# Optimization experiments

Measured on AMD Instinct MI355X. Metric: run time of the kernel, lower is better.

The kernel has to match this reference:

```python
import jax, jax.numpy as jnp
import numpy as np

BETA = 0.25

def setup_inputs() -> dict:
    key = jax.random.key(0)
    k1, k2 = jax.random.split(key)
    z_e = jax.random.normal(k1, (32, 256, 32, 32), dtype=jnp.float32)
    embed_weight = jax.random.normal(k2, (4096, 256), dtype=jnp.float32) * 0.1
    return {"z_e": z_e, "embed_weight": embed_weight}

def reference(z_e, embed_weight):
    # Eval-mode forward (no input noise, no EMA buffer update).
    B, C, H, W = z_e.shape
    K = embed_weight.shape[0]
    z_t = jnp.transpose(z_e, (0, 2, 3, 1))            # [B,H,W,C]
    z_flat = z_t.reshape(-1, C)                        # [N,C]
    # Squared Euclidean distances; argmin is identical to argmin of cdist(p=2).
    d = (
        jnp.sum(z_flat * z_flat, axis=1, keepdims=True)
        - 2.0 * (z_flat @ embed_weight.T)
        + jnp.sum(embed_weight * embed_weight, axis=1)
    )                                                  # [N,K]
    idx = jnp.argmin(d, axis=1)                        # [N]
    # utilization = (#unique codes used) / vocab_size, jit-safe via bincount-style scatter
    counts = jnp.zeros((K,), dtype=jnp.float32).at[idx].add(1.0)
    utilization = jnp.sum(counts > 0).astype(jnp.float32) / K
    z_q = embed_weight[idx].reshape(B, H, W, C)        # [B,H,W,C]
    commitment_loss = jnp.mean((jax.lax.stop_gradient(z_q) - z_t) ** 2) * BETA
    z_q_st = z_t + jax.lax.stop_gradient(z_q - z_t)    # straight-through
    return jnp.transpose(z_q_st, (0, 3, 1, 2)), commitment_loss, utilization
```

## Files before the change

### kernel.cpp

```cpp
#include <hip/hip_runtime.h>
#include <math.h>


#define WGAP 52

using half8 = __attribute__((ext_vector_type(8))) _Float16;
using f32x4 = __attribute__((ext_vector_type(4))) float;

__device__ __forceinline__ void gload_lds16(const void* g, void* l) {
  __builtin_amdgcn_global_load_lds(
      (const __attribute__((address_space(1))) unsigned int*)g,
      (__attribute__((address_space(3))) unsigned int*)l, 16, 0, 0);
}

__device__ __forceinline__ bool lexlt64(double v, int x, double ov, int ox) {
  return (v < ov) || (v == ov && x < ox);
}

__device__ __forceinline__ void ins3k(int key, int& a0, int& a1, int& a2) {
  const int mx0 = max(key, a0);
  a0 = min(key, a0);
  const int mx1 = max(mx0, a1);
  a1 = min(mx0, a1);
  a2 = min(mx1, a2);
}

__device__ __forceinline__ void mrg3k(int& a0, int& a1, int& a2,
                                      int b0, int b1, int b2) {
  const int c0 = min(a0, b0);
  const int x = max(a0, b0);
  const int y = min(a1, b1);
  const int c1 = min(x, y);
  const int z = max(x, y);
  const int ww = min(a2, b2);
  const int c2 = min(z, ww);
  a0 = c0; a1 = c1; a2 = c2;
}

__global__ __launch_bounds__(256) void vq_prep(const float* __restrict__ E,
                                               uint4* __restrict__ Epk,
                                               float* __restrict__ en1024,
                                               int* __restrict__ used,
                                               double* __restrict__ lossSum,
                                               int* __restrict__ candCount,
                                               int* __restrict__ messyCount) {
  const int t = blockIdx.x * 256 + threadIdx.x;
  if (t < 4096) used[t] = 0;
  if (t == 4096) *lossSum = 0.0;
  if (t == 4097) *candCount = 0;
  if (t == 4098) *messyCount = 0;
  const int code = t >> 5, j = t & 31;
  const int rc = code & 63;
  const int khalf = j >> 4, jo = j & 15;
  const float* src = E + (size_t)code * 256 + j * 8;
  union { half8 h; uint4 u; } pk;
  float s = 0.f;
#pragma unroll
  for (int e = 0; e < 8; ++e) {
    const float z = src[e];
    s = fmaf(z, z, s);
    pk.h[e] = (_Float16)(z * 256.0f);
  }
  const size_t g = (size_t)((code >> 6) * 2 + khalf) * 1024 +
                   rc * 16 + (jo ^ (rc & 15));
  Epk[g] = pk.u;
#pragma unroll
  for (int off = 1; off < 32; off <<= 1) s += __shfl_xor(s, off);
  if (j == 0) en1024[code] = s * 1024.0f;
}

__global__ __launch_bounds__(256, 3) void vq_screen(
    const float* __restrict__ Z, const char* __restrict__ Epk,
    const float* __restrict__ en1024,
    int* __restrict__ pk0, int* __restrict__ pk1, int* __restrict__ pk2) {
  __shared__ char lds[49152];
  const int tid = threadIdx.x;
  const int w = tid >> 6, l = tid & 63;
  const int xcd = blockIdx.x & 7, inner = blockIdx.x >> 3;
  const int part = inner % 3;
  const int qg = (inner / 3) * 8 + xcd;
  const int chs = part * 21 + (part > 0 ? 1 : 0);
  const int che = chs + (part == 0 ? 22 : 21);
  const int S = (che - chs) * 2;
  const int qbase = qg * 128;
  const int b = qbase >> 10;
  const int hwq = (qbase & 1023) + w * 32 + (l & 15);

  const float* Zq = Z + (size_t)b * 262144 + hwq;
  half8 ah[2][8];
#pragma unroll
  for (int u = 0; u < 2; ++u)
#pragma unroll
    for (int ks = 0; ks < 8; ++ks) {
      const int c0 = ks * 32 + (l >> 4) * 8;
#pragma unroll
      for (int e = 0; e < 8; ++e)
        ah[u][ks][e] = (_Float16)(Zq[u * 16 + ((size_t)(c0 + e) << 10)] * 256.0f);
    }

  int lo[4];
#pragma unroll
  for (int s = 0; s < 4; ++s)
    lo[s] = (l & 15) * 256 + (((s * 4 + (l >> 4)) ^ (l & 15)) << 4);

  int k0[2][4], k1[2][4], k2[2][4];
#pragma unroll
  for (int u = 0; u < 2; ++u)
#pragma unroll
    for (int r = 0; r < 4; ++r) {
      k0[u][r] = 0x7fffffff; k1[u][r] = 0x7fffffff; k2[u][r] = 0x7fffffff;
    }

  auto stage = [&](int q) {
    const int ss = chs * 2 + q;
    const char* src = Epk + ((size_t)ss << 14) + w * 4096 + l * 16;
    char* dst = lds + (q % 3) * 16384 + w * 4096;
#pragma unroll
    for (int i = 0; i < 4; ++i) gload_lds16(src + i * 1024, dst + i * 1024);
  };
  stage(0);
  stage(1);

  for (int ch = chs; ch < che; ++ch) {
    f32x4 acc[2][4];
#pragma unroll
    for (int u = 0; u < 2; ++u)
#pragma unroll
      for (int t = 0; t < 4; ++t) acc[u][t] = (f32x4){0.f, 0.f, 0.f, 0.f};

#pragma unroll
    for (int sh = 0; sh < 2; ++sh) {
      const int q = (ch - chs) * 2 + sh;
      if (q + 1 < S) {
        asm volatile("s_waitcnt vmcnt(4)" ::: "memory");
      } else {
        asm volatile("s_waitcnt vmcnt(0)" ::: "memory");
      }
      __builtin_amdgcn_s_barrier();
      __builtin_amdgcn_sched_barrier(0);
      if (q + 2 < S) stage(q + 2);
      const char* Lb = lds + (q % 3) * 16384;
      __builtin_amdgcn_s_setprio(1);
#pragma unroll
      for (int s = 0; s < 4; ++s) {
        const int ks = sh * 4 + s;
#pragma unroll
        for (int t = 0; t < 4; ++t) {
          const half8 eh = *(const half8*)(Lb + t * 4096 + lo[s]);
          acc[0][t] = __builtin_amdgcn_mfma_f32_16x16x32_f16(ah[0][ks], eh, acc[0][t], 0, 0, 0);
          acc[1][t] = __builtin_amdgcn_mfma_f32_16x16x32_f16(ah[1][ks], eh, acc[1][t], 0, 0, 0);
        }
      }
      __builtin_amdgcn_s_setprio(0);
    }

    const int cb = ch * 64;
#pragma unroll
    for (int t = 0; t < 4; ++t) {
      const int code = cb + t * 16 + (l & 15);
      const float en = en1024[code];
#pragma unroll
      for (int u = 0; u < 2; ++u)
#pragma unroll
        for (int r = 0; r < 4; ++r) {
          const float df = fmaf(acc[u][t][r], -0.03125f, en);
          const int di = (int)df;
          const int key = (int)(((unsigned)di << 12) + (unsigned)code);
          ins3k(key, k0[u][r], k1[u][r], k2[u][r]);
        }
    }
  }

#pragma unroll
  for (int mask = 1; mask <= 8; mask <<= 1) {
#pragma unroll
    for (int u = 0; u < 2; ++u)
#pragma unroll
      for (int r = 0; r < 4; ++r) {
        const int o0 = __shfl_xor(k0[u][r], mask);
        const int o1 = __shfl_xor(k1[u][r], mask);
        const int o2 = __shfl_xor(k2[u][r], mask);
        mrg3k(k0[u][r], k1[u][r], k2[u][r], o0, o1, o2);
      }
  }
  if ((l & 15) == 0) {
#pragma unroll
    for (int u = 0; u < 2; ++u)
#pragma unroll
      for (int r = 0; r < 4; ++r) {
        const int n = qbase + w * 32 + u * 16 + (l >> 4) * 4 + r;
        const int o = part * 32768 + n;
        pk0[o] = k0[u][r]; pk1[o] = k1[u][r]; pk2[o] = k2[u][r];
      }
  }
}

__global__ __launch_bounds__(256) void vq_merge(
    const int* __restrict__ pk0, const int* __restrict__ pk1,
    const int* __restrict__ pk2, int* __restrict__ idxOut,
    int* __restrict__ cand, int* __restrict__ candCount,
    int* __restrict__ messy, int* __restrict__ messyCount,
    int* __restrict__ pi0, int* __restrict__ pi1, int* __restrict__ pi2) {
  const int n = blockIdx.x * 256 + threadIdx.x;
  int a0 = pk0[n], a1 = pk1[n], a2 = pk2[n];
#pragma unroll
  for (int q = 1; q < 3; ++q) {
    const int o = q * 32768 + n;
    mrg3k(a0, a1, a2, pk0[o], pk1[o], pk2[o]);
  }
  const int x0 = a0 & 0xfff;
  idxOut[n] = x0;
  const int d0 = a0 >> 12, d1 = a1 >> 12, d2 = a2 >> 12;
  if (d1 - d0 < WGAP) {
    if (d2 - d0 < WGAP) {
      const int p = atomicAdd(messyCount, 1);
      if (p < 4096) messy[p] = n;
    } else {
      const int p = atomicAdd(candCount, 1);
      cand[p] = n;
      pi0[n] = x0; pi1[n] = a1 & 0xfff; pi2[n] = a2 & 0xfff;
    }
  }
}

__global__ __launch_bounds__(256) void vq_cand3(
    const float* __restrict__ Z, const float* __restrict__ E,
    const int* __restrict__ pi0, const int* __restrict__ pi1,
    const int* __restrict__ pi2, const int* __restrict__ cand,
    const int* __restrict__ candCount, int* __restrict__ idxOut) {
  const int w = threadIdx.x >> 6, l = threadIdx.x & 63;
  const int cnt = *candCount;
  for (int j = blockIdx.x * 4 + w; j < cnt; j += gridDim.x * 4) {
    const int n = cand[j];
    const int b = n >> 10, hw = n & 1023;
    const int ca = pi0[n], cbn = pi1[n], cc = pi2[n];
    float z4[4];
#pragma unroll
    for (int i = 0; i < 4; ++i)
      z4[i] = Z[(size_t)b * 262144 + ((size_t)(l * 4 + i) << 10) + hw];
    const float4 e0 = *(const float4*)(E + (size_t)ca * 256 + l * 4);
    const float4 e1 = *(const float4*)(E + (size_t)cbn * 256 + l * 4);
    const float4 e2 = *(const float4*)(E + (size_t)cc * 256 + l * 4);
    double d0 = 0, d1 = 0, d2 = 0;
    const float* p0 = (const float*)&e0;
    const float* p1 = (const float*)&e1;
    const float* p2 = (const float*)&e2;
#pragma unroll
    for (int i = 0; i < 4; ++i) {
      const double f0 = (double)z4[i] - (double)p0[i];
      const double f1 = (double)z4[i] - (double)p1[i];
      const double f2 = (double)z4[i] - (double)p2[i];
      d0 = fma(f0, f0, d0);
      d1 = fma(f1, f1, d1);
      d2 = fma(f2, f2, d2);
    }
#pragma unroll
    for (int off = 32; off > 0; off >>= 1) {
      d0 += __shfl_down(d0, off);
      d1 += __shfl_down(d1, off);
      d2 += __shfl_down(d2, off);
    }
    if (l == 0) {
      double bv = d0; int bx = ca;
      if (lexlt64(d1, cbn, bv, bx)) { bv = d1; bx = cbn; }
      if (lexlt64(d2, cc, bv, bx)) { bv = d2; bx = cc; }
      idxOut[n] = bx;
    }
  }
}

__global__ __launch_bounds__(256) void vq_messy1(
    const float* __restrict__ Z, const float* __restrict__ E,
    const int* __restrict__ messy, const int* __restrict__ messyCount,
    double* __restrict__ parv, int* __restrict__ parx) {
  __shared__ float zs[4][256];
  __shared__ double rv[4][256];
  __shared__ int ri[4][256];
  const int cnt0 = *messyCount;
  const int cnt = cnt0 > 4096 ? 4096 : cnt0;
  const int jobs = ((cnt + 3) >> 2) * 16;
  const int t = threadIdx.x;
  for (int job = blockIdx.x; job < jobs; job += gridDim.x) {
    const int grp = job >> 4, chunk = job & 15;
    __syncthreads();
    {
      const int q = t >> 6, lq = t & 63;
      const int mi = grp * 4 + q;
      const int n = messy[mi < cnt ? mi : grp * 4];
      const int b = n >> 10, hw = n & 1023;
#pragma unroll
      for (int i = 0; i < 4; ++i)
        zs[q][lq * 4 + i] =
            Z[(size_t)b * 262144 + ((size_t)(lq * 4 + i) << 10) + hw];
    }
    __syncthreads();
    const int code = chunk * 256 + t;
    const float* er = E + (size_t)code * 256;
    double s0 = 0, s1 = 0, s2 = 0, s3 = 0;
    for (int c = 0; c < 256; ++c) {
      const double ec = (double)er[c];
      const double f0 = (double)zs[0][c] - ec;
      const double f1 = (double)zs[1][c] - ec;
      const double f2 = (double)zs[2][c] - ec;
      const double f3 = (double)zs[3][c] - ec;
      s0 = fma(f0, f0, s0);
      s1 = fma(f1, f1, s1);
      s2 = fma(f2, f2, s2);
      s3 = fma(f3, f3, s3);
    }
    rv[0][t] = s0; rv[1][t] = s1; rv[2][t] = s2; rv[3][t] = s3;
    ri[0][t] = code; ri[1][t] = code; ri[2][t] = code; ri[3][t] = code;
    __syncthreads();
    for (int s = 128; s > 0; s >>= 1) {
      if (t < s) {
#pragma unroll
        for (int qq = 0; qq < 4; ++qq)
          if (lexlt64(rv[qq][t + s], ri[qq][t + s], rv[qq][t], ri[qq][t])) {
            rv[qq][t] = rv[qq][t + s];
            ri[qq][t] = ri[qq][t + s];
          }
      }
      __syncthreads();
    }
    if (t == 0) {
#pragma unroll
      for (int qq = 0; qq < 4; ++qq) {
        const int mi = grp * 4 + qq;
        if (mi < cnt) {
          parv[mi * 16 + chunk] = rv[qq][0];
          parx[mi * 16 + chunk] = ri[qq][0];
        }
      }
    }
  }
}

__global__ __launch_bounds__(256) void vq_messy2(
    const int* __restrict__ messy, const int* __restrict__ messyCount,
    const double* __restrict__ parv, const int* __restrict__ parx,
    int* __restrict__ idxOut) {
  const int cnt0 = *messyCount;
  const int cnt = cnt0 > 4096 ? 4096 : cnt0;
  for (int j = blockIdx.x * 256 + threadIdx.x; j < cnt; j += gridDim.x * 256) {
    double bv = parv[j * 16];
    int bx = parx[j * 16];
    for (int ch = 1; ch < 16; ++ch) {
      const double v = parv[j * 16 + ch];
      const int x = parx[j * 16 + ch];
      if (lexlt64(v, x, bv, bx)) { bv = v; bx = x; }
    }
    idxOut[messy[j]] = bx;
  }
}

__global__ __launch_bounds__(256) void vq_out(
    const float* __restrict__ Z, const float* __restrict__ E,
    const int* __restrict__ idx, float* __restrict__ out,
    double* __restrict__ lossSum, int* __restrict__ used) {
  __shared__ float zt[32][257];
  __shared__ int ids[32];
  const int tid = threadIdx.x;
  const int qb = blockIdx.x * 32;
  const int b = qb >> 10, hw0 = qb & 1023;
  if (tid < 32) {
    const int id = idx[qb + tid];
    ids[tid] = id;
    used[id] = 1;
  }
  __syncthreads();
  const int w = tid >> 6, l = tid & 63;
#pragma unroll
  for (int rr = 0; rr < 8; ++rr) {
    const int q = rr * 4 + w;
    const float4 v = *(const float4*)(E + (size_t)ids[q] * 256 + l * 4);
    zt[q][l * 4 + 0] = v.x;
    zt[q][l * 4 + 1] = v.y;
    zt[q][l * 4 + 2] = v.z;
    zt[q][l * 4 + 3] = v.w;
  }
  __syncthreads();
  const int hwl = tid & 31, cc = tid >> 5;
  const float* Zb = Z + (size_t)b * 262144 + hw0 + hwl;
  float* Ob = out + (size_t)b * 262144 + hw0 + hwl;
  float ls = 0.f;
#pragma unroll 4
  for (int it = 0; it < 32; ++it) {
    const int c = it * 8 + cc;
    const float o = zt[hwl][c];
    const float z = Zb[(size_t)c << 10];
    Ob[(size_t)c << 10] = o;
    const float d = o - z;
    ls = fmaf(d, d, ls);
  }
#pragma unroll
  for (int off = 32; off > 0; off >>= 1) ls += __shfl_down(ls, off);
  __shared__ float red[4];
  if (l == 0) red[w] = ls;
  __syncthreads();
  if (tid == 0)
    atomicAdd(lossSum, (double)((red[0] + red[1]) + (red[2] + red[3])));
}

__global__ __launch_bounds__(256) void vq_final(const int* __restrict__ used,
                                                const double* __restrict__ lossSum,
                                                float* __restrict__ out) {
  __shared__ int cnt[256];
  int c = 0;
  for (int k = threadIdx.x; k < 4096; k += 256) c += (used[k] > 0);
  cnt[threadIdx.x] = c;
  __syncthreads();
  if (threadIdx.x == 0) {
    int tot = 0;
    for (int t = 0; t < 256; ++t) tot += cnt[t];
    out[8388608] = (float)(*lossSum * 0.25 / 8388608.0);
    out[8388609] = (float)tot / 4096.0f;
  }
}

extern "C" void kernel_launch(void* const* d_in, const int* in_sizes, int n_in,
                              void* d_out, int out_size, void* d_ws, size_t ws_size,
                              hipStream_t stream) {
  const float* Z = (const float*)d_in[0];
  const float* E = (const float*)d_in[1];
  float* out = (float*)d_out;
  char* w = (char*)d_ws;

  int* idx = (int*)w;
  int* cand = (int*)(w + 131072);
  float* en1024 = (float*)(w + 262144);
  int* used = (int*)(w + 278528);
  double* lossSum = (double*)(w + 294912);
  int* candCount = (int*)(w + 294920);
  int* messyCount = (int*)(w + 294924);

  char* Epk16 = (char*)out;
  int* pk0 = (int*)(out + 524288);
  int* pk1 = (int*)(out + 655360);
  int* pk2 = (int*)(out + 786432);
  int* pi0 = (int*)(out + 917504);
  int* pi1 = (int*)(out + 950272);
  int* pi2 = (int*)(out + 983040);
  int* messy = (int*)(out + 1015808);
  double* parv = (double*)(out + 1019904);
  int* parx = (int*)(out + 1150976);

  vq_prep<<<512, 256, 0, stream>>>(E, (uint4*)Epk16, en1024, used, lossSum,
                                   candCount, messyCount);
  vq_screen<<<768, 256, 0, stream>>>(Z, Epk16, en1024, pk0, pk1, pk2);
  vq_merge<<<128, 256, 0, stream>>>(pk0, pk1, pk2, idx, cand, candCount,
                                    messy, messyCount, pi0, pi1, pi2);
  vq_cand3<<<256, 256, 0, stream>>>(Z, E, pi0, pi1, pi2, cand, candCount, idx);
  vq_messy1<<<512, 256, 0, stream>>>(Z, E, messy, messyCount, parv, parx);
  vq_messy2<<<8, 256, 0, stream>>>(messy, messyCount, parv, parx, idx);
  vq_out<<<1024, 256, 0, stream>>>(Z, E, idx, out, lossSum, used);
  vq_final<<<1, 256, 0, stream>>>(used, lossSum, out);
}
```

Measured before the change: 180.1 us.

## Fuse exact-recheck kernels and fold final reduction into last-block epilogue

```diff
diff --git a/kernel.cpp b/kernel.cpp
--- a/kernel.cpp
+++ b/kernel.cpp
@@ -43,12 +43,16 @@
                                                int* __restrict__ used,
                                                double* __restrict__ lossSum,
                                                int* __restrict__ candCount,
-                                               int* __restrict__ messyCount) {
+                                               int* __restrict__ messyCount,
+                                               int* __restrict__ syncCnt,
+                                               int* __restrict__ outCnt) {
   const int t = blockIdx.x * 256 + threadIdx.x;
   if (t < 4096) used[t] = 0;
   if (t == 4096) *lossSum = 0.0;
   if (t == 4097) *candCount = 0;
   if (t == 4098) *messyCount = 0;
+  if (t == 4099) *syncCnt = 0;
+  if (t == 4100) *outCnt = 0;
   const int code = t >> 5, j = t & 31;
   const int rc = code & 63;
   const int khalf = j >> 4, jo = j & 15;
@@ -111,15 +115,17 @@
       k0[u][r] = 0x7fffffff; k1[u][r] = 0x7fffffff; k2[u][r] = 0x7fffffff;
     }
 
-  auto stage = [&](int q) {
+  auto stage = [&](int q, int slot) {
     const int ss = chs * 2 + q;
     const char* src = Epk + ((size_t)ss << 14) + w * 4096 + l * 16;
-    char* dst = lds + (q % 3) * 16384 + w * 4096;
+    char* dst = lds + slot * 16384 + w * 4096;
 #pragma unroll
     for (int i = 0; i < 4; ++i) gload_lds16(src + i * 1024, dst + i * 1024);
   };
-  stage(0);
-  stage(1);
+  stage(0, 0);
+  stage(1, 1);
+  int cur = 0;
+  int pf = 2;
 
   for (int ch = chs; ch < che; ++ch) {
     f32x4 acc[2][4];
@@ -132,14 +138,12 @@
     for (int sh = 0; sh < 2; ++sh) {
       const int q = (ch - chs) * 2 + sh;
       if (q + 1 < S) {
-        asm volatile("s_waitcnt vmcnt(4)" ::: "memory");
+        asm volatile("s_waitcnt vmcnt(4)\n\ts_barrier" ::: "memory");
       } else {
-        asm volatile("s_waitcnt vmcnt(0)" ::: "memory");
-      }
-      __builtin_amdgcn_s_barrier();
-      __builtin_amdgcn_sched_barrier(0);
-      if (q + 2 < S) stage(q + 2);
-      const char* Lb = lds + (q % 3) * 16384;
+        asm volatile("s_waitcnt vmcnt(0)\n\ts_barrier" ::: "memory");
+      }
+      if (q + 2 < S) stage(q + 2, pf);
+      const char* Lb = lds + cur * 16384;
       __builtin_amdgcn_s_setprio(1);
 #pragma unroll
       for (int s = 0; s < 4; ++s) {
@@ -152,6 +156,8 @@
         }
       }
       __builtin_amdgcn_s_setprio(0);
+      cur = (cur == 2) ? 0 : cur + 1;
+      pf = (pf == 2) ? 0 : pf + 1;
     }
 
     const int cb = ch * 64;
@@ -223,12 +229,17 @@
   }
 }
 
-__global__ __launch_bounds__(256) void vq_cand3(
+__global__ __launch_bounds__(256) void vq_exact(
     const float* __restrict__ Z, const float* __restrict__ E,
     const int* __restrict__ pi0, const int* __restrict__ pi1,
     const int* __restrict__ pi2, const int* __restrict__ cand,
-    const int* __restrict__ candCount, int* __restrict__ idxOut) {
-  const int w = threadIdx.x >> 6, l = threadIdx.x & 63;
+    const int* __restrict__ candCount, const int* __restrict__ messy,
+    const int* __restrict__ messyCount, double* __restrict__ parv,
+    int* __restrict__ parx, int* __restrict__ idxOut,
+    int* __restrict__ syncCnt) {
+  const int t = threadIdx.x;
+  const int w = t >> 6, l = t & 63;
+
   const int cnt = *candCount;
   for (int j = blockIdx.x * 4 + w; j < cnt; j += gridDim.x * 4) {
     const int n = cand[j];
@@ -267,26 +278,20 @@
       idxOut[n] = bx;
     }
   }
-}
-
-__global__ __launch_bounds__(256) void vq_messy1(
-    const float* __restrict__ Z, const float* __restrict__ E,
-    const int* __restrict__ messy, const int* __restrict__ messyCount,
-    double* __restrict__ parv, int* __restrict__ parx) {
+
   __shared__ float zs[4][256];
   __shared__ double rv[4][256];
   __shared__ int ri[4][256];
-  const int cnt0 = *messyCount;
-  const int cnt = cnt0 > 4096 ? 4096 : cnt0;
-  const int jobs = ((cnt + 3) >> 2) * 16;
-  const int t = threadIdx.x;
+  const int mcnt0 = *messyCount;
+  const int mcnt = mcnt0 > 4096 ? 4096 : mcnt0;
+  const int jobs = ((mcnt + 3) >> 2) * 16;
   for (int job = blockIdx.x; job < jobs; job += gridDim.x) {
     const int grp = job >> 4, chunk = job & 15;
     __syncthreads();
     {
       const int q = t >> 6, lq = t & 63;
       const int mi = grp * 4 + q;
-      const int n = messy[mi < cnt ? mi : grp * 4];
+      const int n = messy[mi < mcnt ? mi : grp * 4];
       const int b = n >> 10, hw = n & 1023;
 #pragma unroll
       for (int i = 0; i < 4; ++i)
@@ -326,37 +331,41 @@
 #pragma unroll
       for (int qq = 0; qq < 4; ++qq) {
         const int mi = grp * 4 + qq;
-        if (mi < cnt) {
+        if (mi < mcnt) {
           parv[mi * 16 + chunk] = rv[qq][0];
           parx[mi * 16 + chunk] = ri[qq][0];
         }
       }
     }
   }
-}
-
-__global__ __launch_bounds__(256) void vq_messy2(
-    const int* __restrict__ messy, const int* __restrict__ messyCount,
-    const double* __restrict__ parv, const int* __restrict__ parx,
-    int* __restrict__ idxOut) {
-  const int cnt0 = *messyCount;
-  const int cnt = cnt0 > 4096 ? 4096 : cnt0;
-  for (int j = blockIdx.x * 256 + threadIdx.x; j < cnt; j += gridDim.x * 256) {
-    double bv = parv[j * 16];
-    int bx = parx[j * 16];
-    for (int ch = 1; ch < 16; ++ch) {
-      const double v = parv[j * 16 + ch];
-      const int x = parx[j * 16 + ch];
-      if (lexlt64(v, x, bv, bx)) { bv = v; bx = x; }
-    }
-    idxOut[messy[j]] = bx;
+
+  __shared__ int lastFlag;
+  __syncthreads();
+  if (t == 0) {
+    __threadfence();
+    lastFlag = (atomicAdd(syncCnt, 1) == (int)gridDim.x - 1);
+  }
+  __syncthreads();
+  if (lastFlag) {
+    __threadfence();
+    for (int j = t; j < mcnt; j += 256) {
+      double bv = parv[j * 16];
+      int bx = parx[j * 16];
+      for (int ch = 1; ch < 16; ++ch) {
+        const double v = parv[j * 16 + ch];
+        const int x = parx[j * 16 + ch];
+        if (lexlt64(v, x, bv, bx)) { bv = v; bx = x; }
+      }
+      idxOut[messy[j]] = bx;
+    }
   }
 }
 
 __global__ __launch_bounds__(256) void vq_out(
     const float* __restrict__ Z, const float* __restrict__ E,
     const int* __restrict__ idx, float* __restrict__ out,
-    double* __restrict__ lossSum, int* __restrict__ used) {
+    double* __restrict__ lossSum, int* __restrict__ used,
+    int* __restrict__ outCnt) {
   __shared__ float zt[32][257];
   __shared__ int ids[32];
   const int tid = threadIdx.x;
@@ -399,21 +408,27 @@
   __syncthreads();
   if (tid == 0)
     atomicAdd(lossSum, (double)((red[0] + red[1]) + (red[2] + red[3])));
-}
-
-__global__ __launch_bounds__(256) void vq_final(const int* __restrict__ used,
-                                                const double* __restrict__ lossSum,
-                                                float* __restrict__ out) {
-  __shared__ int cnt[256];
-  int c = 0;
-  for (int k = threadIdx.x; k < 4096; k += 256) c += (used[k] > 0);
-  cnt[threadIdx.x] = c;
-  __syncthreads();
-  if (threadIdx.x == 0) {
-    int tot = 0;
-    for (int t = 0; t < 256; ++t) tot += cnt[t];
-    out[8388608] = (float)(*lossSum * 0.25 / 8388608.0);
-    out[8388609] = (float)tot / 4096.0f;
+
+  __shared__ int lastO;
+  __syncthreads();
+  if (tid == 0) {
+    __threadfence();
+    lastO = (atomicAdd(outCnt, 1) == (int)gridDim.x - 1);
+  }
+  __syncthreads();
+  if (lastO) {
+    __threadfence();
+    __shared__ int cnt[256];
+    int c = 0;
+    for (int k = tid; k < 4096; k += 256) c += (used[k] > 0);
+    cnt[tid] = c;
+    __syncthreads();
+    if (tid == 0) {
+      int tot = 0;
+      for (int u = 0; u < 256; ++u) tot += cnt[u];
+      out[8388608] = (float)(*lossSum * 0.25 / 8388608.0);
+      out[8388609] = (float)tot / 4096.0f;
+    }
   }
 }
 
@@ -432,6 +447,8 @@
   double* lossSum = (double*)(w + 294912);
   int* candCount = (int*)(w + 294920);
   int* messyCount = (int*)(w + 294924);
+  int* syncCnt = (int*)(w + 294928);
+  int* outCnt = (int*)(w + 294932);
 
   char* Epk16 = (char*)out;
   int* pk0 = (int*)(out + 524288);
@@ -445,13 +462,11 @@
   int* parx = (int*)(out + 1150976);
 
   vq_prep<<<512, 256, 0, stream>>>(E, (uint4*)Epk16, en1024, used, lossSum,
-                                   candCount, messyCount);
+                                   candCount, messyCount, syncCnt, outCnt);
   vq_screen<<<768, 256, 0, stream>>>(Z, Epk16, en1024, pk0, pk1, pk2);
   vq_merge<<<128, 256, 0, stream>>>(pk0, pk1, pk2, idx, cand, candCount,
                                     messy, messyCount, pi0, pi1, pi2);
-  vq_cand3<<<256, 256, 0, stream>>>(Z, E, pi0, pi1, pi2, cand, candCount, idx);
-  vq_messy1<<<512, 256, 0, stream>>>(Z, E, messy, messyCount, parv, parx);
-  vq_messy2<<<8, 256, 0, stream>>>(messy, messyCount, parv, parx, idx);
-  vq_out<<<1024, 256, 0, stream>>>(Z, E, idx, out, lossSum, used);
-  vq_final<<<1, 256, 0, stream>>>(used, lossSum, out);
-}
+  vq_exact<<<768, 256, 0, stream>>>(Z, E, pi0, pi1, pi2, cand, candCount,
+                                    messy, messyCount, parv, parx, idx, syncCnt);
+  vq_out<<<1024, 256, 0, stream>>>(Z, E, idx, out, lossSum, used, outCnt);
+}
```

After: 209.0 us. +16.0%, slower.
